# Performance work log

Measured on AMD Instinct MI355X. Metric: run time of the kernel, lower is better.

Reference implementation:

```python
import jax, jax.numpy as jnp
import numpy as np


def setup_inputs() -> dict:
    key = jax.random.key(0)
    B, L, H, D = 8, 1024, 16, 64
    total_N = B * L
    qkv = jax.random.normal(key, (total_N, 3, H, D), dtype=jnp.float32)
    cu_seqlens = (jnp.arange(B + 1) * L).astype(jnp.int32)  # [B+1] cumulative lengths
    return {"qkv": qkv, "cu_seqlens": cu_seqlens, "max_seqlen": L}


def reference(qkv, cu_seqlens, max_seqlen):
    # qkv: [total_N, 3, H, D]; cu_seqlens: [B+1] int32
    total_N, _, H, D = qkv.shape
    scale = float(D) ** -0.5  # default softmax_scale = 1/sqrt(D)
    q, k, v = qkv[:, 0], qkv[:, 1], qkv[:, 2]  # each [total_N, H, D]

    starts = cu_seqlens[:-1]  # [B]
    ends = cu_seqlens[1:]     # [B]
    # Gather each ragged sequence into a padded [B, L, H, D] layout.
    pos = starts[:, None] + jnp.arange(max_seqlen, dtype=cu_seqlens.dtype)  # [B, L]
    valid = pos < ends[:, None]                                            # [B, L]
    idx = jnp.minimum(pos, total_N - 1)
    qp = q[idx]  # [B, L, H, D]
    kp = k[idx]
    vp = v[idx]

    # Per-sequence non-causal attention, softmax over keys of the same sequence.
    scores = jnp.einsum('bqhd,bkhd->bhqk', qp, kp) * scale  # [B, H, L, L]
    scores = jnp.where(valid[:, None, None, :], scores, jnp.float32(-1e30))
    attn = jax.nn.softmax(scores, axis=-1)
    outp = jnp.einsum('bhqk,bkhd->bqhd', attn, vp)  # [B, L, H, D]
    outp = outp * valid[:, :, None, None].astype(outp.dtype)  # zero padded queries

    # Scatter back to packed layout (invalid slots contribute zeros).
    out = jnp.zeros((total_N, H, D), dtype=qkv.dtype)
    out = out.at[idx.reshape(-1)].add(outp.reshape(-1, H, D))
    return out
```

## Files before the change

### kernel.cpp

```cpp
#include <hip/hip_runtime.h>


typedef __attribute__((ext_vector_type(4))) float f32x4;
typedef __attribute__((ext_vector_type(8))) __bf16 bf16x8;
typedef __attribute__((ext_vector_type(4))) unsigned short us4;
typedef __attribute__((ext_vector_type(8))) unsigned short us8;

#if __has_builtin(__builtin_amdgcn_exp2f)
#define EXP2F __builtin_amdgcn_exp2f
#else
#define EXP2F exp2f
#endif
#if __has_builtin(__builtin_amdgcn_rcpf)
#define RCPF __builtin_amdgcn_rcpf
#else
#define RCPF(x) (1.0f / (x))
#endif

#define LSTR 72
#define K_OFF 0
#define P_OFF (64 * LSTR)
#define VT_OFF (P_OFF + 128 * LSTR)
#define SMEM_USHORTS (VT_OFF + 80 * LSTR)

__device__ __forceinline__ unsigned short f2bf(float x) {
  unsigned u = __builtin_bit_cast(unsigned, x);
  return (unsigned short)((u + 0x8000u) >> 16);
}

__launch_bounds__(256, 4)
__global__ void vla_fa_kernel(const float* __restrict__ qkv,
                              const int* __restrict__ cu,
                              float* __restrict__ out,
                              int B, int nflat) {
  __shared__ __align__(16) unsigned short smem[SMEM_USHORTS];
  const int tid = threadIdx.x;
  const int wave = tid >> 6, lane = tid & 63;
  const int lm = lane & 15, lq = lane >> 4;

  for (int i = tid; i < 16 * LSTR; i += 256) smem[VT_OFF + 64 * LSTR + i] = 0x3F80;

  const int BH = B * 16;
  for (int flat = blockIdx.x; flat < nflat; flat += gridDim.x) {
    const int b = flat % B;
    const int h = (flat / B) & 15;
    const int qb = flat / BH;
    const int s0 = cu[b], s1 = cu[b + 1];
    const int len = s1 - s0;
    if (qb * 128 >= len) continue;
    const int tmax = s1 - 1;

    __syncthreads();

    const float fs = 0.18033688011112042f;
#pragma unroll
    for (int p = 0; p < 8; ++p) {
      int idx = p * 256 + tid;
      int row = idx >> 4, c4 = idx & 15;
      int tok = s0 + qb * 128 + row;
      tok = tok > tmax ? tmax : tok;
      float4 v = *(const float4*)(qkv + (size_t)tok * 3072 + h * 64 + c4 * 4);
      us4 w = {f2bf(v.x * fs), f2bf(v.y * fs), f2bf(v.z * fs), f2bf(v.w * fs)};
      *(us4*)&smem[P_OFF + row * LSTR + c4 * 4] = w;
    }
    __syncthreads();

    bf16x8 qf[2][2];
#pragma unroll
    for (int rt = 0; rt < 2; ++rt)
#pragma unroll
      for (int ks = 0; ks < 2; ++ks)
        qf[rt][ks] = __builtin_bit_cast(
            bf16x8,
            *(const us8*)&smem[P_OFF + (wave * 32 + rt * 16 + lm) * LSTR + ks * 32 + lq * 8]);

    f32x4 Oacc[2][4];
    f32x4 lacc[2];
#pragma unroll
    for (int rt = 0; rt < 2; ++rt) {
      lacc[rt] = f32x4{0.f, 0.f, 0.f, 0.f};
#pragma unroll
      for (int dt = 0; dt < 4; ++dt) Oacc[rt][dt] = f32x4{0.f, 0.f, 0.f, 0.f};
    }

    const int nkt = (len + 63) >> 6;
    for (int kt = 0; kt < nkt; ++kt) {
      __syncthreads();

      const int kbase = kt * 64;
#pragma unroll
      for (int p = 0; p < 4; ++p) {
        int idx = p * 256 + tid;
        int row = idx >> 4, c4 = idx & 15;
        int tok = s0 + kbase + row;
        tok = tok > tmax ? tmax : tok;
        float4 v = *(const float4*)(qkv + (size_t)tok * 3072 + 1024 + h * 64 + c4 * 4);
        us4 w = {f2bf(v.x), f2bf(v.y), f2bf(v.z), f2bf(v.w)};
        *(us4*)&smem[K_OFF + row * LSTR + c4 * 4] = w;
      }
#pragma unroll
      for (int cc = 0; cc < 4; ++cc) {
        int c = wave * 4 + cc;
        float vv[4];
#pragma unroll
        for (int t = 0; t < 4; ++t) {
          int tok = s0 + kbase + c + t * 16;
          tok = tok > tmax ? tmax : tok;
          vv[t] = qkv[(size_t)tok * 3072 + 2048 + h * 64 + lane];
        }
        us4 w = {f2bf(vv[0]), f2bf(vv[1]), f2bf(vv[2]), f2bf(vv[3])};
        *(us4*)&smem[VT_OFF + lane * LSTR + c * 4] = w;
      }
      __syncthreads();

      const bool partial = (len - kbase) < 64;
      f32x4 S[2][4];
#pragma unroll
      for (int rt = 0; rt < 2; ++rt)
#pragma unroll
        for (int nt = 0; nt < 4; ++nt) S[rt][nt] = f32x4{0.f, 0.f, 0.f, 0.f};
#pragma unroll
      for (int ks = 0; ks < 2; ++ks) {
        bf16x8 kfl[4];
#pragma unroll
        for (int nt = 0; nt < 4; ++nt)
          kfl[nt] = __builtin_bit_cast(
              bf16x8, *(const us8*)&smem[K_OFF + (nt * 16 + lm) * LSTR + ks * 32 + lq * 8]);
#pragma unroll
        for (int nt = 0; nt < 4; ++nt)
#pragma unroll
          for (int rt = 0; rt < 2; ++rt)
            S[rt][nt] =
                __builtin_amdgcn_mfma_f32_16x16x32_bf16(qf[rt][ks], kfl[nt], S[rt][nt], 0, 0, 0);
      }
#pragma unroll
      for (int rt = 0; rt < 2; ++rt) {
        if (partial) {
#pragma unroll
          for (int nt = 0; nt < 4; ++nt)
            if (kbase + nt * 16 + lm >= len)
              S[rt][nt] = f32x4{-1e30f, -1e30f, -1e30f, -1e30f};
        }
        int pbase = P_OFF + (wave * 32 + rt * 16 + lq * 4) * LSTR + lm * 4;
#pragma unroll
        for (int r = 0; r < 4; ++r) {
          us4 w = {f2bf(EXP2F(S[rt][0][r])), f2bf(EXP2F(S[rt][1][r])),
                   f2bf(EXP2F(S[rt][2][r])), f2bf(EXP2F(S[rt][3][r]))};
          *(us4*)&smem[pbase + r * LSTR] = w;
        }
      }
      asm volatile("" ::: "memory");

#pragma unroll
      for (int ks = 0; ks < 2; ++ks) {
        bf16x8 vf[5];
#pragma unroll
        for (int dt = 0; dt < 5; ++dt)
          vf[dt] = __builtin_bit_cast(
              bf16x8, *(const us8*)&smem[VT_OFF + (dt * 16 + lm) * LSTR + ks * 32 + lq * 8]);
#pragma unroll
        for (int rt = 0; rt < 2; ++rt) {
          bf16x8 pf = __builtin_bit_cast(
              bf16x8,
              *(const us8*)&smem[P_OFF + (wave * 32 + rt * 16 + lm) * LSTR + ks * 32 + lq * 8]);
#pragma unroll
          for (int dt = 0; dt < 4; ++dt)
            Oacc[rt][dt] = __builtin_amdgcn_mfma_f32_16x16x32_bf16(pf, vf[dt], Oacc[rt][dt], 0, 0, 0);
          lacc[rt] = __builtin_amdgcn_mfma_f32_16x16x32_bf16(pf, vf[4], lacc[rt], 0, 0, 0);
        }
      }
    }

    const int rbase = qb * 128 + wave * 32;
#pragma unroll
    for (int rt = 0; rt < 2; ++rt) {
#pragma unroll
      for (int r = 0; r < 4; ++r) {
        int row = rbase + rt * 16 + lq * 4 + r;
        if (row < len) {
          float rl = RCPF(lacc[rt][r]);
          float* op = out + (size_t)(s0 + row) * 1024 + h * 64 + lm;
#pragma unroll
          for (int dt = 0; dt < 4; ++dt) op[dt * 16] = Oacc[rt][dt][r] * rl;
        }
      }
    }
  }
}

extern "C" void kernel_launch(void* const* d_in, const int* in_sizes, int n_in,
                              void* d_out, int out_size, void* d_ws, size_t ws_size,
                              hipStream_t stream) {
  const float* qkv = (const float*)d_in[0];
  const int* cu = (const int*)d_in[1];
  float* out = (float*)d_out;
  int B = in_sizes[1] - 1;
  int total_N = in_sizes[0] / (3 * 16 * 64);
  int qbmax = (total_N + 127) / 128;
  int nflat = B * 16 * qbmax;
  int nb = nflat < 1024 ? nflat : 1024;
  dim3 grid(nb), block(256, 1, 1);
  hipLaunchKernelGGL(vla_fa_kernel, grid, block, 0, stream, qkv, cu, out, B, nflat);
}
```

Measured before the change: 200.7 us.

## Double query tile to 256 rows with 512-thread blocks and packed bf16 conversion

Each block now handles 256 query rows with 8 waves instead of 128 rows with 4 waves. Each K/V tile loaded and converted from global fp32 is therefore shared by twice as many queries, which halves the redundant K/V traffic and conversion work. The per-element fp32→bf16 rounding is replaced by a packed two-value conversion, using the hardware builtin when available or a perm-based fallback. In exchange, LDS use and block size grow, which may lower occupancy and raise barrier cost with 8 waves per sync.

Result: faster. 188.5 us (-6.0%).

```diff
diff --git a/kernel.cpp b/kernel.cpp
--- a/kernel.cpp
+++ b/kernel.cpp
@@ -3,7 +3,6 @@
 
 typedef __attribute__((ext_vector_type(4))) float f32x4;
 typedef __attribute__((ext_vector_type(8))) __bf16 bf16x8;
-typedef __attribute__((ext_vector_type(4))) unsigned short us4;
 typedef __attribute__((ext_vector_type(8))) unsigned short us8;
 
 #if __has_builtin(__builtin_amdgcn_exp2f)
@@ -17,18 +16,24 @@
 #define RCPF(x) (1.0f / (x))
 #endif
 
+__device__ __forceinline__ unsigned pk_bf16(float a, float b) {
+#if __has_builtin(__builtin_amdgcn_cvt_pk_bf16_f32)
+  auto r = __builtin_amdgcn_cvt_pk_bf16_f32(a, b);
+  return __builtin_bit_cast(unsigned, r);
+#else
+  unsigned ra = __builtin_bit_cast(unsigned, a) + 0x8000u;
+  unsigned rb = __builtin_bit_cast(unsigned, b) + 0x8000u;
+  return __builtin_amdgcn_perm(rb, ra, 0x07060302u);
+#endif
+}
+
 #define LSTR 72
 #define K_OFF 0
 #define P_OFF (64 * LSTR)
-#define VT_OFF (P_OFF + 128 * LSTR)
+#define VT_OFF (P_OFF + 256 * LSTR)
 #define SMEM_USHORTS (VT_OFF + 80 * LSTR)
 
-__device__ __forceinline__ unsigned short f2bf(float x) {
-  unsigned u = __builtin_bit_cast(unsigned, x);
-  return (unsigned short)((u + 0x8000u) >> 16);
-}
-
-__launch_bounds__(256, 4)
+__launch_bounds__(512, 4)
 __global__ void vla_fa_kernel(const float* __restrict__ qkv,
                               const int* __restrict__ cu,
                               float* __restrict__ out,
@@ -38,7 +43,7 @@
   const int wave = tid >> 6, lane = tid & 63;
   const int lm = lane & 15, lq = lane >> 4;
 
-  for (int i = tid; i < 16 * LSTR; i += 256) smem[VT_OFF + 64 * LSTR + i] = 0x3F80;
+  for (int i = tid; i < 16 * LSTR; i += 512) smem[VT_OFF + 64 * LSTR + i] = 0x3F80;
 
   const int BH = B * 16;
   for (int flat = blockIdx.x; flat < nflat; flat += gridDim.x) {
@@ -47,7 +52,7 @@
     const int qb = flat / BH;
     const int s0 = cu[b], s1 = cu[b + 1];
     const int len = s1 - s0;
-    if (qb * 128 >= len) continue;
+    if (qb * 256 >= len) continue;
     const int tmax = s1 - 1;
 
     __syncthreads();
@@ -55,13 +60,13 @@
     const float fs = 0.18033688011112042f;
 #pragma unroll
     for (int p = 0; p < 8; ++p) {
-      int idx = p * 256 + tid;
+      int idx = p * 512 + tid;
       int row = idx >> 4, c4 = idx & 15;
-      int tok = s0 + qb * 128 + row;
+      int tok = s0 + qb * 256 + row;
       tok = tok > tmax ? tmax : tok;
       float4 v = *(const float4*)(qkv + (size_t)tok * 3072 + h * 64 + c4 * 4);
-      us4 w = {f2bf(v.x * fs), f2bf(v.y * fs), f2bf(v.z * fs), f2bf(v.w * fs)};
-      *(us4*)&smem[P_OFF + row * LSTR + c4 * 4] = w;
+      uint2 w = {pk_bf16(v.x * fs, v.y * fs), pk_bf16(v.z * fs, v.w * fs)};
+      *(uint2*)&smem[P_OFF + row * LSTR + c4 * 4] = w;
     }
     __syncthreads();
 
@@ -89,18 +94,18 @@
 
       const int kbase = kt * 64;
 #pragma unroll
-      for (int p = 0; p < 4; ++p) {
-        int idx = p * 256 + tid;
+      for (int p = 0; p < 2; ++p) {
+        int idx = p * 512 + tid;
         int row = idx >> 4, c4 = idx & 15;
         int tok = s0 + kbase + row;
         tok = tok > tmax ? tmax : tok;
         float4 v = *(const float4*)(qkv + (size_t)tok * 3072 + 1024 + h * 64 + c4 * 4);
-        us4 w = {f2bf(v.x), f2bf(v.y), f2bf(v.z), f2bf(v.w)};
-        *(us4*)&smem[K_OFF + row * LSTR + c4 * 4] = w;
-      }
-#pragma unroll
-      for (int cc = 0; cc < 4; ++cc) {
-        int c = wave * 4 + cc;
+        uint2 w = {pk_bf16(v.x, v.y), pk_bf16(v.z, v.w)};
+        *(uint2*)&smem[K_OFF + row * LSTR + c4 * 4] = w;
+      }
+#pragma unroll
+      for (int cc = 0; cc < 2; ++cc) {
+        int c = wave * 2 + cc;
         float vv[4];
 #pragma unroll
         for (int t = 0; t < 4; ++t) {
@@ -108,8 +113,8 @@
           tok = tok > tmax ? tmax : tok;
           vv[t] = qkv[(size_t)tok * 3072 + 2048 + h * 64 + lane];
         }
-        us4 w = {f2bf(vv[0]), f2bf(vv[1]), f2bf(vv[2]), f2bf(vv[3])};
-        *(us4*)&smem[VT_OFF + lane * LSTR + c * 4] = w;
+        uint2 w = {pk_bf16(vv[0], vv[1]), pk_bf16(vv[2], vv[3])};
+        *(uint2*)&smem[VT_OFF + lane * LSTR + c * 4] = w;
       }
       __syncthreads();
 
@@ -144,9 +149,9 @@
         int pbase = P_OFF + (wave * 32 + rt * 16 + lq * 4) * LSTR + lm * 4;
 #pragma unroll
         for (int r = 0; r < 4; ++r) {
-          us4 w = {f2bf(EXP2F(S[rt][0][r])), f2bf(EXP2F(S[rt][1][r])),
-                   f2bf(EXP2F(S[rt][2][r])), f2bf(EXP2F(S[rt][3][r]))};
-          *(us4*)&smem[pbase + r * LSTR] = w;
+          uint2 w = {pk_bf16(EXP2F(S[rt][0][r]), EXP2F(S[rt][1][r])),
+                     pk_bf16(EXP2F(S[rt][2][r]), EXP2F(S[rt][3][r]))};
+          *(uint2*)&smem[pbase + r * LSTR] = w;
         }
       }
       asm volatile("" ::: "memory");
@@ -171,7 +176,7 @@
       }
     }
 
-    const int rbase = qb * 128 + wave * 32;
+    const int rbase = qb * 256 + wave * 32;
 #pragma unroll
     for (int rt = 0; rt < 2; ++rt) {
 #pragma unroll
@@ -196,9 +201,9 @@
   float* out = (float*)d_out;
   int B = in_sizes[1] - 1;
   int total_N = in_sizes[0] / (3 * 16 * 64);
-  int qbmax = (total_N + 127) / 128;
+  int qbmax = (total_N + 255) / 256;
   int nflat = B * 16 * qbmax;
-  int nb = nflat < 1024 ? nflat : 1024;
-  dim3 grid(nb), block(256, 1, 1);
+  int nb = nflat < 512 ? nflat : 512;
+  dim3 grid(nb), block(512, 1, 1);
   hipLaunchKernelGGL(vla_fa_kernel, grid, block, 0, stream, qkv, cu, out, B, nflat);
 }
```
